# Optimization experiments

Hardware: AMD Instinct MI355X
Metric: run time of the kernel (lower is better)

Reference implementation:

```python
import jax, jax.numpy as jnp
import numpy as np

WS = 16          # window_size
HS = 8           # halo_size
NH = 4           # num_heads
DIM = 128
WSH = WS + 2 * HS  # 32, window with halo
B, H, W = 2, 128, 128


def _rel_pos_index():
    # static relative-position index table, (WSH^2, WSH^2), int
    r = np.arange(-HS, WS + HS)
    coords = np.stack(np.meshgrid(r, r, indexing='ij'))        # (2, WSH, WSH)
    cf = coords.reshape(2, -1)                                  # (2, WSH^2)
    rel = (cf[:, :, None] - cf[:, None, :]).transpose(1, 2, 0)  # (L, L, 2)
    rel = rel.copy()
    rel[..., 0] += WS + HS - 1
    rel[..., 1] += WS + HS - 1
    rel[..., 0] *= 2 * WS + 2 * HS - 1
    return rel.sum(-1)  # (1024, 1024)

_RPI = _rel_pos_index()


def setup_inputs() -> dict:
    key = jax.random.key(0)
    ks = jax.random.split(key, 10)
    p = lambda k, shp: (jax.random.normal(k, shp, dtype=jnp.float32) * 0.02)
    return {
        'x': jax.random.normal(ks[0], (B, H, W, DIM), dtype=jnp.float32),
        'Wq': p(ks[1], (DIM, DIM)), 'bq': jnp.zeros((DIM,), jnp.float32),
        'Wk': p(ks[2], (DIM, DIM)), 'bk': jnp.zeros((DIM,), jnp.float32),
        'Wv': p(ks[3], (DIM, DIM)), 'bv': jnp.zeros((DIM,), jnp.float32),
        'Wp': p(ks[4], (DIM, DIM)), 'bp': jnp.zeros((DIM,), jnp.float32),
        'bias_table': p(ks[5], ((2 * WS + 2 * HS - 1) ** 2, NH)),
        'shift_size': 0,
    }


def reference(x, Wq, bq, Wk, bk, Wv, bv, Wp, bp, bias_table, shift_size):
    Bx, Hx, Wx, C = x.shape
    hd = C // NH
    scale = hd ** -0.5
    if shift_size > 0:
        x = jnp.roll(x, (-shift_size, -shift_size), axis=(1, 2))
    # reflect-pad by halo and gather overlapping 32x32 windows (stride 16)
    xp = jnp.pad(x, ((0, 0), (HS, HS), (HS, HS), (0, 0)), mode='reflect')
    nWh, nWw = Hx // WS, Wx // WS
    rows = (jnp.arange(nWh) * WS)[:, None] + jnp.arange(WSH)   # (nWh, 32)
    cols = (jnp.arange(nWw) * WS)[:, None] + jnp.arange(WSH)   # (nWw, 32)
    w = xp[:, rows]                 # (B, nWh, 32, Wp, C)
    w = w[:, :, :, cols]            # (B, nWh, 32, nWw, 32, C)
    w = w.transpose(0, 1, 3, 2, 4, 5).reshape(-1, WSH, WSH, C)  # (B*nW, 32, 32, C)
    center = w[:, HS:HS + WS, HS:HS + WS].reshape(-1, WS * WS, C)   # (nWb, 256, C)
    kv = w.reshape(-1, WSH * WSH, C)                                # (nWb, 1024, C)
    q = (center @ Wq.T + bq).reshape(-1, WS * WS, NH, hd).transpose(0, 2, 1, 3)
    k = (kv @ Wk.T + bk).reshape(-1, WSH * WSH, NH, hd).transpose(0, 2, 1, 3)
    v = (kv @ Wv.T + bv).reshape(-1, WSH * WSH, NH, hd).transpose(0, 2, 1, 3)
    attn = jnp.einsum('bhqd,bhkd->bhqk', q, k) * scale   # (nWb, H, 256, 1024)
    bias = bias_table[_RPI.reshape(-1)].reshape(WSH * WSH, WSH * WSH, NH)
    bias = bias.transpose(2, 0, 1)                        # (H, 1024, 1024)
    start = HS * 2 * WS                                   # 256, as in source
    attn = attn + bias[:, start:start + WS * WS, :][None]
    attn = jax.nn.softmax(attn, axis=-1)
    out = jnp.einsum('bhqk,bhkd->bhqd', attn, v)
    out = out.transpose(0, 2, 1, 3).reshape(-1, WS * WS, C)
    out = out @ Wp.T + bp
    out = out.reshape(Bx, nWh, nWw, WS, WS, C).transpose(0, 1, 3, 2, 4, 5)
    out = out.reshape(Bx, Hx, Wx, C)
    if shift_size > 0:
        out = jnp.roll(out, (shift_size, shift_size), axis=(1, 2))
    return out
```

## Files before the change

kernel.cpp:

```cpp
#include <hip/hip_runtime.h>


typedef unsigned short ushort_t;
typedef __attribute__((ext_vector_type(8))) short bf16x8;
typedef __attribute__((ext_vector_type(4))) float floatx4;

#define NHEADS 4
#define BTBL 2209
#define PK 40
#define VK 72
#define QS_LOG2E 0.2550348635f
#define LOG2E 1.4426950408889634f

#if __has_builtin(__builtin_amdgcn_exp2f)
#define EXP2F(x) __builtin_amdgcn_exp2f(x)
#else
#define EXP2F(x) __expf((x) * 0.6931471805599453f)
#endif

__device__ __forceinline__ int reflect_idx(int p) {
    p = (p < 0) ? -p : p;
    p = (p > 127) ? 254 - p : p;
    return p;
}

__device__ __forceinline__ unsigned f2b(float x) {
    unsigned u = __float_as_uint(x);
    return (u + 0x7fffu + ((u >> 16) & 1u)) >> 16;
}

__global__ __launch_bounds__(256) void prep(
    const float* __restrict__ bt,
    const float* __restrict__ Wq, const float* __restrict__ Wk,
    const float* __restrict__ Wv, const float* __restrict__ Wp,
    const float* __restrict__ bq, const float* __restrict__ bk,
    const float* __restrict__ bv, const float* __restrict__ bp,
    ushort_t* __restrict__ bf,
    ushort_t* __restrict__ Wqkv, ushort_t* __restrict__ Wpb,
    float* __restrict__ bqkv, float* __restrict__ bpb)
{
    const int bx = blockIdx.x;
    if (bx < 4096) {
        int idx = bx * 256 + threadIdx.x;
        int reg  = idx & 3;
        int lane = (idx >> 2) & 63;
        int qt   = (idx >> 8) & 15;
        int kt   = (idx >> 12) & 63;
        int h    = idx >> 18;
        int key  = kt * 16 + ((lane >> 4) << 2) + reg;
        int q    = qt * 16 + (lane & 15);
        int kr = key >> 5, kc = key & 31;
        int bidx = ((q >> 5) + 31 - kr) * 47 + (q & 31) - kc + 23;
        if (bidx < 0) bidx += BTBL;
        bf[idx] = (ushort_t)f2b(bt[bidx * NHEADS + h] * LOG2E);
    } else {
        int idx = (bx - 4096) * 256 + threadIdx.x;
        if (idx < 16384)       Wqkv[idx] = (ushort_t)f2b(Wq[idx]);
        else if (idx < 32768)  Wqkv[idx] = (ushort_t)f2b(Wk[idx - 16384]);
        else if (idx < 49152)  Wqkv[idx] = (ushort_t)f2b(Wv[idx - 32768]);
        else if (idx < 65536)  Wpb[idx - 49152] = (ushort_t)f2b(Wp[idx - 49152]);
        else {
            int e = idx - 65536;
            for (int k = e; k < 512; k += 256) {
                if (k < 128)      bqkv[k] = bq[k];
                else if (k < 256) bqkv[k] = bk[k - 128];
                else if (k < 384) bqkv[k] = bv[k - 256];
                else              bpb[k - 384] = bp[k - 384];
            }
        }
    }
}

__global__ __launch_bounds__(256) void gemm_qkv(
    const float* __restrict__ X, const ushort_t* __restrict__ W,
    const float* __restrict__ bias, ushort_t* __restrict__ Y)
{
    __shared__ ushort_t Xs[64 * 136];

    const int t    = threadIdx.x;
    const int wq   = t >> 6;
    const int lane = t & 63;
    const int quad = lane >> 4;
    const int l15  = lane & 15;
    const int m0   = blockIdx.x * 64;
    const int nb   = blockIdx.y;
    const float sc = (nb == 0) ? QS_LOG2E : 1.0f;

    #pragma unroll
    for (int i = 0; i < 8; ++i) {
        int s = t + i * 256;
        int row = s >> 5, c4 = s & 31;
        float4 v = *(const float4*)&X[(size_t)(m0 + row) * 128 + c4 * 4];
        uint2 pk;
        pk.x = f2b(v.x) | (f2b(v.y) << 16);
        pk.y = f2b(v.z) | (f2b(v.w) << 16);
        *(uint2*)&Xs[row * 136 + c4 * 4] = pk;
    }
    __syncthreads();

    floatx4 acc[8];
    #pragma unroll
    for (int nt = 0; nt < 8; ++nt)
        acc[nt] = (floatx4)(bias[nb * 128 + nt * 16 + l15]);

    #pragma unroll
    for (int kc = 0; kc < 4; ++kc) {
        bf16x8 af = *(const bf16x8*)&Xs[(wq * 16 + l15) * 136 + kc * 32 + quad * 8];
        #pragma unroll
        for (int nt = 0; nt < 8; ++nt) {
            bf16x8 bfr = *(const bf16x8*)&W[(size_t)(nb * 128 + nt * 16 + l15) * 128 + kc * 32 + quad * 8];
            acc[nt] = __builtin_amdgcn_mfma_f32_16x16x32_bf16(af, bfr, acc[nt], 0, 0, 0);
        }
    }

    #pragma unroll
    for (int r = 0; r < 4; ++r) {
        int m = m0 + wq * 16 + quad * 4 + r;
        #pragma unroll
        for (int nt = 0; nt < 8; ++nt)
            Y[(size_t)m * 384 + nb * 128 + nt * 16 + l15] = (ushort_t)f2b(acc[nt][r] * sc);
    }
}

__global__ __launch_bounds__(256) void gemm_proj(
    const ushort_t* __restrict__ X, const ushort_t* __restrict__ W,
    const float* __restrict__ bias, float* __restrict__ Y)
{
    __shared__ ushort_t Xs[64 * 136];

    const int t    = threadIdx.x;
    const int wq   = t >> 6;
    const int lane = t & 63;
    const int quad = lane >> 4;
    const int l15  = lane & 15;
    const int m0   = blockIdx.x * 64;

    #pragma unroll
    for (int i = 0; i < 4; ++i) {
        int s = t + i * 256;
        int row = s >> 4, c8 = s & 15;
        *(int4*)&Xs[row * 136 + c8 * 8] = *(const int4*)&X[(size_t)(m0 + row) * 128 + c8 * 8];
    }
    __syncthreads();

    floatx4 acc[8];
    #pragma unroll
    for (int nt = 0; nt < 8; ++nt)
        acc[nt] = (floatx4)(bias[nt * 16 + l15]);

    #pragma unroll
    for (int kc = 0; kc < 4; ++kc) {
        bf16x8 af = *(const bf16x8*)&Xs[(wq * 16 + l15) * 136 + kc * 32 + quad * 8];
        #pragma unroll
        for (int nt = 0; nt < 8; ++nt) {
            bf16x8 bfr = *(const bf16x8*)&W[(size_t)(nt * 16 + l15) * 128 + kc * 32 + quad * 8];
            acc[nt] = __builtin_amdgcn_mfma_f32_16x16x32_bf16(af, bfr, acc[nt], 0, 0, 0);
        }
    }

    #pragma unroll
    for (int r = 0; r < 4; ++r) {
        int m = m0 + wq * 16 + quad * 4 + r;
        #pragma unroll
        for (int nt = 0; nt < 8; ++nt)
            Y[(size_t)m * 128 + nt * 16 + l15] = acc[nt][r];
    }
}

__global__ __launch_bounds__(256, 2) void halo_attn(
    const ushort_t* __restrict__ QKV,
    const ushort_t* __restrict__ biasf,
    ushort_t* __restrict__ O)
{
    __shared__ ushort_t P_lds[4 * 64 * PK];
    __shared__ ushort_t Vt_lds[4 * 32 * VK];

    const int t    = threadIdx.x;
    const int wave = t >> 6;
    const int lane = t & 63;
    const int quad = lane >> 4;
    const int l15  = lane & 15;

    const int x  = blockIdx.x;
    const int tt = x & 7;
    const int w  = x >> 3;
    const int b  = tt >> 2;
    const int wh = ((tt >> 1) & 1) * 4 + (w >> 2);
    const int ww = (tt & 1) * 4 + (w & 3);
    const int head = blockIdx.y;

    bf16x8 qf[4];
    int qpix[4];
    #pragma unroll
    for (int qt = 0; qt < 4; ++qt) {
        int q_abs = wave * 64 + qt * 16 + l15;
        int gy = wh * 16 + (q_abs >> 4), gx = ww * 16 + (q_abs & 15);
        int pix = (b * 128 + gy) * 128 + gx;
        qpix[qt] = pix;
        qf[qt] = *(const bf16x8*)(QKV + (size_t)pix * 384 + head * 32 + quad * 8);
    }

    floatx4 Oa[2][4];
    #pragma unroll
    for (int dt = 0; dt < 2; ++dt)
        #pragma unroll
        for (int qt = 0; qt < 4; ++qt)
            Oa[dt][qt] = (floatx4)0.f;
    float l[4] = {0.f, 0.f, 0.f, 0.f};

    ushort_t* Pw  = P_lds  + wave * 64 * PK;
    ushort_t* Vtw = Vt_lds + wave * 32 * VK;

    for (int c = 0; c < 16; ++c) {
        {
            int keyv = c * 64 + lane;
            int ky = reflect_idx(wh * 16 + (keyv >> 5) - 8);
            int kx = reflect_idx(ww * 16 + (keyv & 31) - 8);
            int pixv = (b * 128 + ky) * 128 + kx;
            const int4* vp4 = (const int4*)(QKV + (size_t)pixv * 384 + 256 + head * 32);
            int4 vw0 = vp4[0], vw1 = vp4[1], vw2 = vp4[2], vw3 = vp4[3];
            const ushort_t* vs0 = (const ushort_t*)&vw0;
            const ushort_t* vs1 = (const ushort_t*)&vw1;
            const ushort_t* vs2 = (const ushort_t*)&vw2;
            const ushort_t* vs3 = (const ushort_t*)&vw3;
            #pragma unroll
            for (int d = 0; d < 8; ++d) {
                Vtw[(d +  0) * VK + lane] = vs0[d];
                Vtw[(d +  8) * VK + lane] = vs1[d];
                Vtw[(d + 16) * VK + lane] = vs2[d];
                Vtw[(d + 24) * VK + lane] = vs3[d];
            }
        }

        bf16x8 kf[4];
        #pragma unroll
        for (int kt = 0; kt < 4; ++kt) {
            int key = c * 64 + kt * 16 + l15;
            int ky = reflect_idx(wh * 16 + (key >> 5) - 8);
            int kx = reflect_idx(ww * 16 + (key & 31) - 8);
            int pixk = (b * 128 + ky) * 128 + kx;
            kf[kt] = *(const bf16x8*)(QKV + (size_t)pixk * 384 + 128 + head * 32 + quad * 8);
        }

        floatx4 S[4][4];
        #pragma unroll
        for (int kt = 0; kt < 4; ++kt) {
            int kt_abs = c * 4 + kt;
            #pragma unroll
            for (int qt = 0; qt < 4; ++qt) {
                int qt_abs = wave * 4 + qt;
                uint2 pk = *(const uint2*)(biasf +
                    ((((size_t)head * 64 + kt_abs) * 16 + qt_abs) * 64 + lane) * 4);
                S[kt][qt][0] = __uint_as_float(pk.x << 16);
                S[kt][qt][1] = __uint_as_float(pk.x & 0xffff0000u);
                S[kt][qt][2] = __uint_as_float(pk.y << 16);
                S[kt][qt][3] = __uint_as_float(pk.y & 0xffff0000u);
            }
        }
        #pragma unroll
        for (int kt = 0; kt < 4; ++kt)
            #pragma unroll
            for (int qt = 0; qt < 4; ++qt)
                S[kt][qt] = __builtin_amdgcn_mfma_f32_16x16x32_bf16(kf[kt], qf[qt], S[kt][qt], 0, 0, 0);

        #pragma unroll
        for (int qt = 0; qt < 4; ++qt) {
            float ls = 0.f;
            #pragma unroll
            for (int kt = 0; kt < 4; ++kt)
                #pragma unroll
                for (int r = 0; r < 4; ++r) {
                    float p = EXP2F(S[kt][qt][r]);
                    S[kt][qt][r] = p;
                    ls += p;
                }
            l[qt] += ls;
        }

        #pragma unroll
        for (int ks = 0; ks < 2; ++ks) {
            #pragma unroll
            for (int qt = 0; qt < 4; ++qt)
                #pragma unroll
                for (int kh = 0; kh < 2; ++kh) {
                    int kt = ks * 2 + kh;
                    uint2 pk;
                    pk.x = __builtin_amdgcn_perm(__float_as_uint(S[kt][qt][1]),
                                                 __float_as_uint(S[kt][qt][0]), 0x07060302u);
                    pk.y = __builtin_amdgcn_perm(__float_as_uint(S[kt][qt][3]),
                                                 __float_as_uint(S[kt][qt][2]), 0x07060302u);
                    *(uint2*)&Pw[(qt * 16 + l15) * PK + kh * 16 + quad * 4] = pk;
                }
            bf16x8 vf[2];
            #pragma unroll
            for (int dt = 0; dt < 2; ++dt)
                vf[dt] = *(const bf16x8*)&Vtw[(dt * 16 + l15) * VK + ks * 32 + quad * 8];
            #pragma unroll
            for (int qt = 0; qt < 4; ++qt) {
                bf16x8 pf = *(const bf16x8*)&Pw[(qt * 16 + l15) * PK + quad * 8];
                #pragma unroll
                for (int dt = 0; dt < 2; ++dt)
                    Oa[dt][qt] = __builtin_amdgcn_mfma_f32_16x16x32_bf16(vf[dt], pf, Oa[dt][qt], 0, 0, 0);
            }
        }
    }

    #pragma unroll
    for (int qt = 0; qt < 4; ++qt) {
        float lq = l[qt];
        lq += __shfl_xor(lq, 16);
        lq += __shfl_xor(lq, 32);
        float inv = 1.0f / lq;
        #pragma unroll
        for (int dt = 0; dt < 2; ++dt) {
            uint2 pk;
            pk.x = f2b(Oa[dt][qt][0] * inv) | (f2b(Oa[dt][qt][1] * inv) << 16);
            pk.y = f2b(Oa[dt][qt][2] * inv) | (f2b(Oa[dt][qt][3] * inv) << 16);
            *(uint2*)(O + (size_t)qpix[qt] * 128 + head * 32 + dt * 16 + quad * 4) = pk;
        }
    }
}

extern "C" void kernel_launch(void* const* d_in, const int* in_sizes, int n_in,
                              void* d_out, int out_size, void* d_ws, size_t ws_size,
                              hipStream_t stream)
{
    const float* x          = (const float*)d_in[0];
    const float* Wq         = (const float*)d_in[1];
    const float* bq         = (const float*)d_in[2];
    const float* Wk         = (const float*)d_in[3];
    const float* bk         = (const float*)d_in[4];
    const float* Wv         = (const float*)d_in[5];
    const float* bv         = (const float*)d_in[6];
    const float* Wp         = (const float*)d_in[7];
    const float* bp         = (const float*)d_in[8];
    const float* bias_table = (const float*)d_in[9];
    float* out = (float*)d_out;

    char* ws = (char*)d_ws;
    ushort_t* Wqkv  = (ushort_t*)(ws);
    ushort_t* Wpb   = (ushort_t*)(ws + 98304);
    float*    bqkv  = (float*)   (ws + 131072);
    float*    bpb   = (float*)   (ws + 132608);
    ushort_t* QKV   = (ushort_t*)(ws + 133120);
    ushort_t* Ob    = (ushort_t*)(ws + 25298944);
    ushort_t* biasf = (ushort_t*)(ws + 33687552);

    prep<<<dim3(4353), dim3(256), 0, stream>>>(bias_table, Wq, Wk, Wv, Wp,
                                               bq, bk, bv, bp,
                                               biasf, Wqkv, Wpb, bqkv, bpb);
    gemm_qkv<<<dim3(512, 3), dim3(256), 0, stream>>>(x, Wqkv, bqkv, QKV);
    halo_attn<<<dim3(128, NHEADS), dim3(256), 0, stream>>>(QKV, biasf, Ob);
    gemm_proj<<<dim3(512), dim3(256), 0, stream>>>(Ob, Wpb, bpb, out);
}
```

Baseline: 188.4 us.

## Fuse weight prep into QKV GEMM, split attention queries across more blocks

Result: slower. 234.1 us (+24.2%).

```diff
diff --git a/kernel.cpp b/kernel.cpp
--- a/kernel.cpp
+++ b/kernel.cpp
@@ -29,19 +29,31 @@
     return (u + 0x7fffu + ((u >> 16) & 1u)) >> 16;
 }
 
-__global__ __launch_bounds__(256) void prep(
+union bf8u { bf16x8 v; unsigned u[4]; };
+
+__device__ __forceinline__ bf16x8 pack8(const float* p) {
+    float4 a = *(const float4*)p;
+    float4 b = *(const float4*)(p + 4);
+    bf8u r;
+    r.u[0] = f2b(a.x) | (f2b(a.y) << 16);
+    r.u[1] = f2b(a.z) | (f2b(a.w) << 16);
+    r.u[2] = f2b(b.x) | (f2b(b.y) << 16);
+    r.u[3] = f2b(b.z) | (f2b(b.w) << 16);
+    return r.v;
+}
+
+__global__ __launch_bounds__(256) void front(
+    const float* __restrict__ X,
+    const float* __restrict__ Wq, const float* __restrict__ Wk,
+    const float* __restrict__ Wv,
+    const float* __restrict__ bq, const float* __restrict__ bk,
+    const float* __restrict__ bv,
     const float* __restrict__ bt,
-    const float* __restrict__ Wq, const float* __restrict__ Wk,
-    const float* __restrict__ Wv, const float* __restrict__ Wp,
-    const float* __restrict__ bq, const float* __restrict__ bk,
-    const float* __restrict__ bv, const float* __restrict__ bp,
-    ushort_t* __restrict__ bf,
-    ushort_t* __restrict__ Wqkv, ushort_t* __restrict__ Wpb,
-    float* __restrict__ bqkv, float* __restrict__ bpb)
+    ushort_t* __restrict__ QKV, ushort_t* __restrict__ biasf)
 {
     const int bx = blockIdx.x;
-    if (bx < 4096) {
-        int idx = bx * 256 + threadIdx.x;
+    if (bx >= 1536) {
+        int idx = (bx - 1536) * 256 + threadIdx.x;
         int reg  = idx & 3;
         int lane = (idx >> 2) & 63;
         int qt   = (idx >> 8) & 15;
@@ -52,29 +64,10 @@
         int kr = key >> 5, kc = key & 31;
         int bidx = ((q >> 5) + 31 - kr) * 47 + (q & 31) - kc + 23;
         if (bidx < 0) bidx += BTBL;
-        bf[idx] = (ushort_t)f2b(bt[bidx * NHEADS + h] * LOG2E);
-    } else {
-        int idx = (bx - 4096) * 256 + threadIdx.x;
-        if (idx < 16384)       Wqkv[idx] = (ushort_t)f2b(Wq[idx]);
-        else if (idx < 32768)  Wqkv[idx] = (ushort_t)f2b(Wk[idx - 16384]);
-        else if (idx < 49152)  Wqkv[idx] = (ushort_t)f2b(Wv[idx - 32768]);
-        else if (idx < 65536)  Wpb[idx - 49152] = (ushort_t)f2b(Wp[idx - 49152]);
-        else {
-            int e = idx - 65536;
-            for (int k = e; k < 512; k += 256) {
-                if (k < 128)      bqkv[k] = bq[k];
-                else if (k < 256) bqkv[k] = bk[k - 128];
-                else if (k < 384) bqkv[k] = bv[k - 256];
-                else              bpb[k - 384] = bp[k - 384];
-            }
-        }
-    }
-}
-
-__global__ __launch_bounds__(256) void gemm_qkv(
-    const float* __restrict__ X, const ushort_t* __restrict__ W,
-    const float* __restrict__ bias, ushort_t* __restrict__ Y)
-{
+        biasf[idx] = (ushort_t)f2b(bt[bidx * NHEADS + h] * LOG2E);
+        return;
+    }
+
     __shared__ ushort_t Xs[64 * 136];
 
     const int t    = threadIdx.x;
@@ -82,8 +75,10 @@
     const int lane = t & 63;
     const int quad = lane >> 4;
     const int l15  = lane & 15;
-    const int m0   = blockIdx.x * 64;
-    const int nb   = blockIdx.y;
+    const int m0   = (bx & 511) * 64;
+    const int nb   = bx >> 9;
+    const float* W    = (nb == 0) ? Wq : ((nb == 1) ? Wk : Wv);
+    const float* bias = (nb == 0) ? bq : ((nb == 1) ? bk : bv);
     const float sc = (nb == 0) ? QS_LOG2E : 1.0f;
 
     #pragma unroll
@@ -101,14 +96,14 @@
     floatx4 acc[8];
     #pragma unroll
     for (int nt = 0; nt < 8; ++nt)
-        acc[nt] = (floatx4)(bias[nb * 128 + nt * 16 + l15]);
+        acc[nt] = (floatx4)(bias[nt * 16 + l15]);
 
     #pragma unroll
     for (int kc = 0; kc < 4; ++kc) {
         bf16x8 af = *(const bf16x8*)&Xs[(wq * 16 + l15) * 136 + kc * 32 + quad * 8];
         #pragma unroll
         for (int nt = 0; nt < 8; ++nt) {
-            bf16x8 bfr = *(const bf16x8*)&W[(size_t)(nb * 128 + nt * 16 + l15) * 128 + kc * 32 + quad * 8];
+            bf16x8 bfr = pack8(&W[(size_t)(nt * 16 + l15) * 128 + kc * 32 + quad * 8]);
             acc[nt] = __builtin_amdgcn_mfma_f32_16x16x32_bf16(af, bfr, acc[nt], 0, 0, 0);
         }
     }
@@ -118,12 +113,12 @@
         int m = m0 + wq * 16 + quad * 4 + r;
         #pragma unroll
         for (int nt = 0; nt < 8; ++nt)
-            Y[(size_t)m * 384 + nb * 128 + nt * 16 + l15] = (ushort_t)f2b(acc[nt][r] * sc);
+            QKV[(size_t)m * 384 + nb * 128 + nt * 16 + l15] = (ushort_t)f2b(acc[nt][r] * sc);
     }
 }
 
 __global__ __launch_bounds__(256) void gemm_proj(
-    const ushort_t* __restrict__ X, const ushort_t* __restrict__ W,
+    const ushort_t* __restrict__ X, const float* __restrict__ W,
     const float* __restrict__ bias, float* __restrict__ Y)
 {
     __shared__ ushort_t Xs[64 * 136];
@@ -134,6 +129,7 @@
     const int quad = lane >> 4;
     const int l15  = lane & 15;
     const int m0   = blockIdx.x * 64;
+    const int n0   = blockIdx.y * 64;
 
     #pragma unroll
     for (int i = 0; i < 4; ++i) {
@@ -143,17 +139,17 @@
     }
     __syncthreads();
 
-    floatx4 acc[8];
-    #pragma unroll
-    for (int nt = 0; nt < 8; ++nt)
-        acc[nt] = (floatx4)(bias[nt * 16 + l15]);
+    floatx4 acc[4];
+    #pragma unroll
+    for (int nt = 0; nt < 4; ++nt)
+        acc[nt] = (floatx4)(bias[n0 + nt * 16 + l15]);
 
     #pragma unroll
     for (int kc = 0; kc < 4; ++kc) {
         bf16x8 af = *(const bf16x8*)&Xs[(wq * 16 + l15) * 136 + kc * 32 + quad * 8];
         #pragma unroll
-        for (int nt = 0; nt < 8; ++nt) {
-            bf16x8 bfr = *(const bf16x8*)&W[(size_t)(nt * 16 + l15) * 128 + kc * 32 + quad * 8];
+        for (int nt = 0; nt < 4; ++nt) {
+            bf16x8 bfr = pack8(&W[(size_t)(n0 + nt * 16 + l15) * 128 + kc * 32 + quad * 8]);
             acc[nt] = __builtin_amdgcn_mfma_f32_16x16x32_bf16(af, bfr, acc[nt], 0, 0, 0);
         }
     }
@@ -162,8 +158,8 @@
     for (int r = 0; r < 4; ++r) {
         int m = m0 + wq * 16 + quad * 4 + r;
         #pragma unroll
-        for (int nt = 0; nt < 8; ++nt)
-            Y[(size_t)m * 128 + nt * 16 + l15] = acc[nt][r];
+        for (int nt = 0; nt < 4; ++nt)
+            Y[(size_t)m * 128 + n0 + nt * 16 + l15] = acc[nt][r];
     }
 }
 
@@ -172,7 +168,7 @@
     const ushort_t* __restrict__ biasf,
     ushort_t* __restrict__ O)
 {
-    __shared__ ushort_t P_lds[4 * 64 * PK];
+    __shared__ ushort_t P_lds[4 * 32 * PK];
     __shared__ ushort_t Vt_lds[4 * 32 * VK];
 
     const int t    = threadIdx.x;
@@ -181,34 +177,36 @@
     const int quad = lane >> 4;
     const int l15  = lane & 15;
 
-    const int x  = blockIdx.x;
-    const int tt = x & 7;
-    const int w  = x >> 3;
-    const int b  = tt >> 2;
-    const int wh = ((tt >> 1) & 1) * 4 + (w >> 2);
-    const int ww = (tt & 1) * 4 + (w & 3);
-    const int head = blockIdx.y;
-
-    bf16x8 qf[4];
-    int qpix[4];
-    #pragma unroll
-    for (int qt = 0; qt < 4; ++qt) {
-        int q_abs = wave * 64 + qt * 16 + l15;
+    const int x     = blockIdx.x;
+    const int tt    = x & 7;
+    const int r     = x >> 3;
+    const int qhalf = r & 1;
+    const int ws    = r >> 1;
+    const int b     = tt >> 2;
+    const int wh    = ((tt >> 1) & 1) * 4 + (ws >> 2);
+    const int ww    = (tt & 1) * 4 + (ws & 3);
+    const int head  = blockIdx.y;
+
+    bf16x8 qf[2];
+    int qpix[2];
+    #pragma unroll
+    for (int qt = 0; qt < 2; ++qt) {
+        int q_abs = qhalf * 128 + wave * 32 + qt * 16 + l15;
         int gy = wh * 16 + (q_abs >> 4), gx = ww * 16 + (q_abs & 15);
         int pix = (b * 128 + gy) * 128 + gx;
         qpix[qt] = pix;
         qf[qt] = *(const bf16x8*)(QKV + (size_t)pix * 384 + head * 32 + quad * 8);
     }
 
-    floatx4 Oa[2][4];
+    floatx4 Oa[2][2];
     #pragma unroll
     for (int dt = 0; dt < 2; ++dt)
         #pragma unroll
-        for (int qt = 0; qt < 4; ++qt)
+        for (int qt = 0; qt < 2; ++qt)
             Oa[dt][qt] = (floatx4)0.f;
-    float l[4] = {0.f, 0.f, 0.f, 0.f};
-
-    ushort_t* Pw  = P_lds  + wave * 64 * PK;
+    float l[2] = {0.f, 0.f};
+
+    ushort_t* Pw  = P_lds  + wave * 32 * PK;
     ushort_t* Vtw = Vt_lds + wave * 32 * VK;
 
     for (int c = 0; c < 16; ++c) {
@@ -242,13 +240,13 @@
             kf[kt] = *(const bf16x8*)(QKV + (size_t)pixk * 384 + 128 + head * 32 + quad * 8);
         }
 
-        floatx4 S[4][4];
+        floatx4 S[4][2];
         #pragma unroll
         for (int kt = 0; kt < 4; ++kt) {
             int kt_abs = c * 4 + kt;
             #pragma unroll
-            for (int qt = 0; qt < 4; ++qt) {
-                int qt_abs = wave * 4 + qt;
+            for (int qt = 0; qt < 2; ++qt) {
+                int qt_abs = qhalf * 8 + wave * 2 + qt;
                 uint2 pk = *(const uint2*)(biasf +
                     ((((size_t)head * 64 + kt_abs) * 16 + qt_abs) * 64 + lane) * 4);
                 S[kt][qt][0] = __uint_as_float(pk.x << 16);
@@ -260,18 +258,18 @@
         #pragma unroll
         for (int kt = 0; kt < 4; ++kt)
             #pragma unroll
-            for (int qt = 0; qt < 4; ++qt)
+            for (int qt = 0; qt < 2; ++qt)
                 S[kt][qt] = __builtin_amdgcn_mfma_f32_16x16x32_bf16(kf[kt], qf[qt], S[kt][qt], 0, 0, 0);
 
         #pragma unroll
-        for (int qt = 0; qt < 4; ++qt) {
+        for (int qt = 0; qt < 2; ++qt) {
             float ls = 0.f;
             #pragma unroll
             for (int kt = 0; kt < 4; ++kt)
                 #pragma unroll
-                for (int r = 0; r < 4; ++r) {
-                    float p = EXP2F(S[kt][qt][r]);
-                    S[kt][qt][r] = p;
+                for (int r2 = 0; r2 < 4; ++r2) {
+                    float p = EXP2F(S[kt][qt][r2]);
+                    S[kt][qt][r2] = p;
                     ls += p;
                 }
             l[qt] += ls;
@@ -280,7 +278,7 @@
         #pragma unroll
         for (int ks = 0; ks < 2; ++ks) {
             #pragma unroll
-            for (int qt = 0; qt < 4; ++qt)
+            for (int qt = 0; qt < 2; ++qt)
                 #pragma unroll
                 for (int kh = 0; kh < 2; ++kh) {
                     int kt = ks * 2 + kh;
@@ -296,7 +294,7 @@
             for (int dt = 0; dt < 2; ++dt)
                 vf[dt] = *(const bf16x8*)&Vtw[(dt * 16 + l15) * VK + ks * 32 + quad * 8];
             #pragma unroll
-            for (int qt = 0; qt < 4; ++qt) {
+            for (int qt = 0; qt < 2; ++qt) {
                 bf16x8 pf = *(const bf16x8*)&Pw[(qt * 16 + l15) * PK + quad * 8];
                 #pragma unroll
                 for (int dt = 0; dt < 2; ++dt)
@@ -306,7 +304,7 @@
     }
 
     #pragma unroll
-    for (int qt = 0; qt < 4; ++qt) {
+    for (int qt = 0; qt < 2; ++qt) {
         float lq = l[qt];
         lq += __shfl_xor(lq, 16);
         lq += __shfl_xor(lq, 32);
@@ -338,18 +336,12 @@
     float* out = (float*)d_out;
 
     char* ws = (char*)d_ws;
-    ushort_t* Wqkv  = (ushort_t*)(ws);
-    ushort_t* Wpb   = (ushort_t*)(ws + 98304);
-    float*    bqkv  = (float*)   (ws + 131072);
-    float*    bpb   = (float*)   (ws + 132608);
-    ushort_t* QKV   = (ushort_t*)(ws + 133120);
-    ushort_t* Ob    = (ushort_t*)(ws + 25298944);
-    ushort_t* biasf = (ushort_t*)(ws + 33687552);
-
-    prep<<<dim3(4353), dim3(256), 0, stream>>>(bias_table, Wq, Wk, Wv, Wp,
-                                               bq, bk, bv, bp,
-                                               biasf, Wqkv, Wpb, bqkv, bpb);
-    gemm_qkv<<<dim3(512, 3), dim3(256), 0, stream>>>(x, Wqkv, bqkv, QKV);
-    halo_attn<<<dim3(128, NHEADS), dim3(256), 0, stream>>>(QKV, biasf, Ob);
-    gemm_proj<<<dim3(512), dim3(256), 0, stream>>>(Ob, Wpb, bpb, out);
-}
+    ushort_t* QKV   = (ushort_t*)(ws);
+    ushort_t* Ob    = (ushort_t*)(ws + 25165824);
+    ushort_t* biasf = (ushort_t*)(ws + 33554432);
+
+    front<<<dim3(5632), dim3(256), 0, stream>>>(x, Wq, Wk, Wv, bq, bk, bv,
+                                                bias_table, QKV, biasf);
+    halo_attn<<<dim3(256, NHEADS), dim3(256), 0, stream>>>(QKV, biasf, Ob);
+    gemm_proj<<<dim3(512, 2), dim3(256), 0, stream>>>(Ob, Wp, bp, out);
+}
```
